# Performance work log

Measured on AMD Instinct MI355X. Metric: run time of the kernel, lower is better.

Reference implementation:

```python
import jax, jax.numpy as jnp
import numpy as np

B = 2048
G = 8
C = B * G  # 16384


def setup_inputs() -> dict:
    key = jax.random.key(0)
    k1, k2 = jax.random.split(key)
    student_scores = jax.random.normal(k1, (B, C), dtype=jnp.float32)
    teacher_targets = jax.random.uniform(k2, (B, G), dtype=jnp.float32)
    return {
        "student_scores": student_scores,
        "teacher_targets": teacher_targets,
        "group_size": G,
    }


def reference(student_scores, teacher_targets, group_size):
    b = student_scores.shape[0]
    rows = jnp.arange(b)
    labels = rows * group_size  # base target column per row
    neg = jnp.finfo(student_scores.dtype).min
    mask = jnp.zeros_like(student_scores)
    loss = jnp.zeros((), dtype=student_scores.dtype)
    # group_size is small and fixed (e.g. 8): Python loop over it is fine.
    for i in range(group_size):
        tgt = labels + i                       # [B]
        s = student_scores + mask              # [B, C], previously-used targets masked to -inf
        lse = jax.nn.logsumexp(s, axis=-1)     # [B]
        picked = s[rows, tgt]                  # [B] logits at the current target
        ce = lse - picked                      # per-row cross entropy, reduction='none'
        loss = loss + jnp.mean(teacher_targets[:, i] * ce)
        mask = mask.at[rows, tgt].set(neg)
    return loss
```

## Files before the change

### kernel.cpp

```cpp
#include <hip/hip_runtime.h>


#define BB 2048
#define CC 16384
#define GG 8
#define NT 512
#define PER_THREAD (CC / NT)
#define NVEC (PER_THREAD / 4)

typedef float f32x4 __attribute__((ext_vector_type(4)));

__global__ __launch_bounds__(NT, 8) void kd_row_kernel(
    const float* __restrict__ scores,
    const float* __restrict__ teacher,
    float* __restrict__ partial)
{
    const int row = blockIdx.x;
    const int tid = threadIdx.x;
    const float* rp = scores + (size_t)row * CC;
    const f32x4* rp4 = reinterpret_cast<const f32x4*>(rp);

    __shared__ float sh_t[GG], sh_w[GG];
    if (tid < GG) {
        sh_t[tid] = rp[row * GG + tid];
        sh_w[tid] = teacher[row * GG + tid];
    }

    f32x4 v[NVEC];
#pragma unroll
    for (int i = 0; i < NVEC; ++i) v[i] = rp4[i * NT + tid];

    __builtin_amdgcn_sched_barrier(0);

    float s = 0.0f;
#pragma unroll
    for (int i = 0; i < NVEC; ++i)
        s += __expf(v[i].x) + __expf(v[i].y) + __expf(v[i].z) + __expf(v[i].w);

#pragma unroll
    for (int off = 32; off >= 1; off >>= 1) s += __shfl_xor(s, off);

    __shared__ float ss[NT / 64];
    const int wave = tid >> 6;
    const int lane = tid & 63;
    if (lane == 0) ss[wave] = s;
    __syncthreads();

    if (tid == 0) {
        float S = 0.0f;
#pragma unroll
        for (int w = 0; w < NT / 64; ++w) S += ss[w];

        float contrib = 0.0f;
        float S2 = S;
#pragma unroll
        for (int i = 0; i < GG; ++i) {
            contrib += sh_w[i] * (__logf(S2) - sh_t[i]);
            S2 -= __expf(sh_t[i]);
        }
        partial[row] = contrib;
    }
}

__global__ __launch_bounds__(256) void kd_reduce_kernel(
    const float* __restrict__ partial,
    float* __restrict__ out)
{
    const int tid = threadIdx.x;
    float s = 0.0f;
#pragma unroll
    for (int j = 0; j < BB / 256; ++j) s += partial[j * 256 + tid];
#pragma unroll
    for (int off = 32; off >= 1; off >>= 1) s += __shfl_xor(s, off);
    __shared__ float ws[4];
    const int wave = tid >> 6;
    const int lane = tid & 63;
    if (lane == 0) ws[wave] = s;
    __syncthreads();
    if (tid == 0) out[0] = (ws[0] + ws[1] + ws[2] + ws[3]) * (1.0f / BB);
}

extern "C" void kernel_launch(void* const* d_in, const int* in_sizes, int n_in,
                              void* d_out, int out_size, void* d_ws, size_t ws_size,
                              hipStream_t stream) {
    const float* scores  = (const float*)d_in[0];
    const float* teacher = (const float*)d_in[1];
    float* partial = (float*)d_ws;
    float* out = (float*)d_out;

    kd_row_kernel<<<BB, NT, 0, stream>>>(scores, teacher, partial);
    kd_reduce_kernel<<<1, 256, 0, stream>>>(partial, out);
}
```

Baseline: 27.17 us.

## Halve block size, batch row loads, parallelize group tail across lanes

Each row block now uses 256 threads instead of 512 and processes its 16 vec4 loads per thread in two batches of 8, using two accumulators for the exp sums. The sequential 8-step epilogue on thread 0 is replaced by a prefix scan and reduction across 8 lanes with shuffles. The reduce kernel reads partials as vec4 loads. The aim is to cut the serial tail and lower per-block overhead and register pressure, at the cost of fewer loads in flight per batch.

```diff
diff --git a/kernel.cpp b/kernel.cpp
--- a/kernel.cpp
+++ b/kernel.cpp
@@ -4,9 +4,10 @@
 #define BB 2048
 #define CC 16384
 #define GG 8
-#define NT 512
+#define NT 256
 #define PER_THREAD (CC / NT)
-#define NVEC (PER_THREAD / 4)
+#define NBATCH 2
+#define NVEC 8
 
 typedef float f32x4 __attribute__((ext_vector_type(4)));
 
@@ -20,22 +21,26 @@
     const float* rp = scores + (size_t)row * CC;
     const f32x4* rp4 = reinterpret_cast<const f32x4*>(rp);
 
-    __shared__ float sh_t[GG], sh_w[GG];
+    float t = 0.0f, w = 0.0f;
     if (tid < GG) {
-        sh_t[tid] = rp[row * GG + tid];
-        sh_w[tid] = teacher[row * GG + tid];
+        t = rp[row * GG + tid];
+        w = teacher[row * GG + tid];
     }
 
+    float s0 = 0.0f, s1 = 0.0f;
     f32x4 v[NVEC];
 #pragma unroll
-    for (int i = 0; i < NVEC; ++i) v[i] = rp4[i * NT + tid];
-
-    __builtin_amdgcn_sched_barrier(0);
-
-    float s = 0.0f;
+    for (int b = 0; b < NBATCH; ++b) {
 #pragma unroll
-    for (int i = 0; i < NVEC; ++i)
-        s += __expf(v[i].x) + __expf(v[i].y) + __expf(v[i].z) + __expf(v[i].w);
+        for (int i = 0; i < NVEC; ++i) v[i] = rp4[(b * NVEC + i) * NT + tid];
+        __builtin_amdgcn_sched_barrier(0);
+#pragma unroll
+        for (int i = 0; i < NVEC; ++i) {
+            s0 += __expf(v[i].x) + __expf(v[i].y);
+            s1 += __expf(v[i].z) + __expf(v[i].w);
+        }
+    }
+    float s = s0 + s1;
 
 #pragma unroll
     for (int off = 32; off >= 1; off >>= 1) s += __shfl_xor(s, off);
@@ -46,19 +51,24 @@
     if (lane == 0) ss[wave] = s;
     __syncthreads();
 
-    if (tid == 0) {
+    if (tid < GG) {
         float S = 0.0f;
 #pragma unroll
-        for (int w = 0; w < NT / 64; ++w) S += ss[w];
+        for (int q = 0; q < NT / 64; ++q) S += ss[q];
 
-        float contrib = 0.0f;
-        float S2 = S;
+        float e = __expf(t);
+        float p = e;
 #pragma unroll
-        for (int i = 0; i < GG; ++i) {
-            contrib += sh_w[i] * (__logf(S2) - sh_t[i]);
-            S2 -= __expf(sh_t[i]);
+        for (int off = 1; off < GG; off <<= 1) {
+            float o = __shfl_up(p, off, GG);
+            if (tid >= off) p += o;
         }
-        partial[row] = contrib;
+        float S2 = S - (p - e);
+        float contrib = w * (__logf(S2) - t);
+#pragma unroll
+        for (int off = GG / 2; off >= 1; off >>= 1)
+            contrib += __shfl_xor(contrib, off, GG);
+        if (tid == 0) partial[row] = contrib;
     }
 }
 
@@ -67,9 +77,10 @@
     float* __restrict__ out)
 {
     const int tid = threadIdx.x;
-    float s = 0.0f;
-#pragma unroll
-    for (int j = 0; j < BB / 256; ++j) s += partial[j * 256 + tid];
+    const f32x4* p4 = reinterpret_cast<const f32x4*>(partial);
+    f32x4 a = p4[tid];
+    f32x4 b = p4[tid + 256];
+    float s = (a.x + a.y + a.z + a.w) + (b.x + b.y + b.z + b.w);
 #pragma unroll
     for (int off = 32; off >= 1; off >>= 1) s += __shfl_xor(s, off);
     __shared__ float ws[4];
```

Measured after the change: 26.52 us. -2.4%, faster.
